# Kernel tuning notes

Hardware: AMD Instinct MI355X
Metric: run time of the kernel (lower is better)

Reference implementation:

```python
import jax, jax.numpy as jnp
import numpy as np

BOUND = 3.0
MIN_BIN_W = 1e-3   # min_bin_width
MIN_BIN_H = 1e-3   # min_bin_height
MIN_DERIV = 1e-3   # min_derivative
MIN_LAMBDA = 0.025
EPS = 1e-6


def _knots(frac, min_size, left, right):
    # frac: [D, K] normalized (softmax) bin fractions -> (bin sizes [D,K], knot positions [D,K+1])
    K = frac.shape[-1]
    sizes = min_size + (1.0 - min_size * K) * frac
    cum = jnp.cumsum(sizes, axis=-1)
    cum = jnp.concatenate([jnp.zeros_like(cum[..., :1]), cum], axis=-1)
    cum = (right - left) * cum + left
    cum = cum.at[..., 0].set(left)
    cum = cum.at[..., -1].set(right)
    sizes = cum[..., 1:] - cum[..., :-1]
    return sizes, cum


def _spline_fwd(x, uw, uh, ud, ul, bound=BOUND):
    # x: [B, D]; uw/uh/ul: [D, K]; ud: [D, K-1]
    B, D = x.shape
    K = uw.shape[-1]
    w = jax.nn.softmax(uw, axis=-1)
    h = jax.nn.softmax(uh, axis=-1)
    d = MIN_DERIV + jax.nn.softplus(ud)
    lam = MIN_LAMBDA + (1.0 - 2.0 * MIN_LAMBDA) * jax.nn.sigmoid(ul)

    left, right = -bound, bound
    widths, cumwidths = _knots(w, MIN_BIN_W, left, right)
    heights, cumheights = _knots(h, MIN_BIN_H, left, right)
    ones = jnp.ones_like(d[..., :1])
    derivs = jnp.concatenate([ones, d, ones], axis=-1)  # [D, K+1]; identity slope at the tails

    inside = (x >= left) & (x <= right)
    xc = jnp.clip(x, left, right)  # keep spline branch NaN-free for outside points

    # bucketize: index of bin containing each input, per dimension  -> [B, D]
    bin_idx = jnp.sum(xc[..., None] >= (cumwidths + EPS)[None], axis=-1) - 1
    bin_idx = jnp.clip(bin_idx, 0, K - 1)

    def sel(t):
        # gather per-(sample, dim) bin parameter: t [D, K or K+1] -> [B, D]
        tb = jnp.broadcast_to(t[None], (B,) + t.shape)
        return jnp.take_along_axis(tb, bin_idx[..., None], axis=-1)[..., 0]

    iw, icw = sel(widths), sel(cumwidths)
    ih, ich = sel(heights), sel(cumheights)
    idelta = sel(heights / widths)
    d0, d1 = sel(derivs), sel(derivs[..., 1:])
    il = sel(lam)

    # monotonic *linear* rational spline (Dolatabadi et al.), forward direction
    wa = 1.0
    wb = jnp.sqrt(d0 / d1) * wa
    wc = (il * wa * d0 + (1.0 - il) * wb * d1) / idelta
    ya = ich
    yb = ih + ich
    yc = ((1.0 - il) * wa * ya + il * wb * yb) / ((1.0 - il) * wa + il * wb)

    theta = (xc - icw) / iw
    lo = theta <= il
    num = jnp.where(lo,
                    wa * ya * (il - theta) + wc * yc * theta,
                    wc * yc * (1.0 - theta) + wb * yb * (theta - il))
    den = jnp.where(lo,
                    wa * (il - theta) + wc * theta,
                    wc * (1.0 - theta) + wb * (theta - il))
    dnum = jnp.where(lo,
                     wa * wc * il * (yc - ya),
                     wb * wc * (1.0 - il) * (yb - yc)) / iw

    u = jnp.where(inside, num / den, x)                      # identity outside the box
    logabsdet = jnp.where(inside, jnp.log(dnum) - 2.0 * jnp.log(jnp.abs(den)), 0.0)
    return u, jnp.sum(logabsdet, axis=1)


def setup_inputs() -> dict:
    B, D, K = 32768, 256, 32
    key = jax.random.key(0)
    k1, k2, k3, k4, k5 = jax.random.split(key, 5)
    return {
        "x": jax.random.normal(k1, (B, D), jnp.float32),
        "uw": jax.random.normal(k2, (D, K), jnp.float32),
        "uh": jax.random.normal(k3, (D, K), jnp.float32),
        "ud": jax.random.normal(k4, (D, K - 1), jnp.float32),
        "ul": jax.random.uniform(k5, (D, K), jnp.float32),
    }


def reference(x, uw, uh, ud, ul):
    # f: data x -> latent u, plus log|det J| summed over feature dim
    return _spline_fwd(x, uw, uh, ud, ul)
```

## Files before the change

### kernel.cpp

```cpp
#include <hip/hip_runtime.h>
#include <hip/hip_fp16.h>
#include <math.h>
#include <stdint.h>

#define D_DIM 256
#define K_BINS 32
#define NCELL 1024
#define ENT_DW 8
#define ENT_STRIDE 260
#define LIC_STRIDE 34
#define LUT_BSTRIDE 1028
#define SLICE 16

static constexpr float BOUND = 3.0f;
static constexpr float MIN_BIN_W = 1e-3f;
static constexpr float MIN_DERIV = 1e-3f;
static constexpr float MIN_LAMBDA = 0.025f;
static constexpr float EPS_ = 1e-6f;
static constexpr float CELL_W = 6.0f / NCELL;
static constexpr float CELL_S = NCELL / 6.0f;
static constexpr float LN2_ = 0.69314718055994531f;

__device__ __forceinline__ float softplusf_(float x) {
  return fmaxf(x, 0.0f) + log1pf(expf(-fabsf(x)));
}

__device__ __forceinline__ float pack2h_as_f32(float a, float b) {
  __half2 h = __halves2half2(__float2half_rn(a), __float2half_rn(b));
  union { __half2 h; uint32_t u; } c;
  c.h = h;
  return __uint_as_float(c.u);
}

__device__ __forceinline__ float2 unpack2h_from_f32(float v) {
  union { uint32_t u; __half2 h; } c;
  c.u = __float_as_uint(v);
  return make_float2(__low2float(c.h), __high2float(c.h));
}

__device__ __forceinline__ float dpp_rowsum16(float v) {
  int t;
  t = __builtin_amdgcn_update_dpp(0, __float_as_int(v), 0x128, 0xF, 0xF, false);
  v += __int_as_float(t);
  t = __builtin_amdgcn_update_dpp(0, __float_as_int(v), 0x124, 0xF, 0xF, false);
  v += __int_as_float(t);
  t = __builtin_amdgcn_update_dpp(0, __float_as_int(v), 0x122, 0xF, 0xF, false);
  v += __int_as_float(t);
  t = __builtin_amdgcn_update_dpp(0, __float_as_int(v), 0x121, 0xF, 0xF, false);
  v += __int_as_float(t);
  return v;
}

__global__ __launch_bounds__(512) void spline_fused(
    const float* __restrict__ x,
    const float* __restrict__ uw,
    const float* __restrict__ uh,
    const float* __restrict__ ud,
    const float* __restrict__ ul,
    float* __restrict__ uout,
    float* __restrict__ part,
    int B) {
  __shared__ float lent[SLICE * ENT_STRIDE];
  __shared__ float lic[SLICE * LIC_STRIDE];
  __shared__ uint8_t lutb[SLICE * LUT_BSTRIDE];

  int tid = threadIdx.x;
  int slice = blockIdx.x & 15;
  int group = blockIdx.x >> 4;
  int d0 = slice * SLICE;

  {
    int k = tid & 31;
    int dim = tid >> 5;
    int d = d0 + dim;

    float uwv = uw[d * K_BINS + k];
    float uhv = uh[d * K_BINS + k];
    float ulv = ul[d * K_BINS + k];
    float udv = (k < K_BINS - 1) ? ud[d * (K_BINS - 1) + k] : 0.0f;

    float wm = uwv, hm = uhv;
    for (int o = 16; o; o >>= 1) {
      wm = fmaxf(wm, __shfl_xor(wm, o, 32));
      hm = fmaxf(hm, __shfl_xor(hm, o, 32));
    }
    float ew = expf(uwv - wm), eh = expf(uhv - hm);
    float ws = ew, hs = eh;
    for (int o = 16; o; o >>= 1) {
      ws += __shfl_xor(ws, o, 32);
      hs += __shfl_xor(hs, o, 32);
    }
    const float kfac = 1.0f - MIN_BIN_W * (float)K_BINS;
    float sw = MIN_BIN_W + kfac * (ew / ws);
    float sh = MIN_BIN_W + kfac * (eh / hs);

    float cws = sw, chs = sh;
    for (int o = 1; o < 32; o <<= 1) {
      float tw = __shfl_up(cws, o, 32);
      float th = __shfl_up(chs, o, 32);
      if (k >= o) { cws += tw; chs += th; }
    }
    const float scale = 2.0f * BOUND;
    float raw_w = scale * cws - BOUND;
    float raw_h = scale * chs - BOUND;
    float upw = __shfl_up(raw_w, 1, 32);
    float uph = __shfl_up(raw_h, 1, 32);
    float cw_lo = (k == 0) ? -BOUND : upw;
    float ch_lo = (k == 0) ? -BOUND : uph;
    float cw_hi = (k == K_BINS - 1) ? BOUND : raw_w;
    float ch_hi = (k == K_BINS - 1) ? BOUND : raw_h;

    float iw = cw_hi - cw_lo;
    float ih = ch_hi - ch_lo;

    float dk = MIN_DERIV + softplusf_(udv);
    float dprev = __shfl_up(dk, 1, 32);
    float d1 = (k == K_BINS - 1) ? 1.0f : dk;
    float dd0 = (k == 0) ? 1.0f : dprev;

    float sg = 1.0f / (1.0f + expf(-ulv));
    float lam = MIN_LAMBDA + (1.0f - 2.0f * MIN_LAMBDA) * sg;

    float wb = sqrtf(dd0 / d1);
    float delta = ih / iw;
    float wc = (lam * dd0 + (1.0f - lam) * wb * d1) / delta;
    float denom = (1.0f - lam) + lam * wb;
    float dyc = lam * wb * ih / denom;
    float dyb = ih - dyc;
    float ya = ch_lo;
    float inv_iw = 1.0f / iw;
    float yc = ya + dyc;

    float* e = &lent[dim * ENT_STRIDE + k * ENT_DW];
    e[0] = cw_lo;
    e[1] = inv_iw;
    e[2] = lam;
    e[3] = wc;
    e[4] = wb;
    e[5] = yc;
    e[6] = pack2h_as_f32(dyc, dyb);
    e[7] = pack2h_as_f32(log2f(wc * lam * dyc * inv_iw),
                         log2f(wc * wb * (1.0f - lam) * dyb * inv_iw));

    float t = cw_lo + EPS_;
    lic[dim * LIC_STRIDE + k] = t;
    if (k == 0) lic[dim * LIC_STRIDE + 32] = 1e30f;

    int c0 = 0;
    if (k > 0) {
      float q = (t + BOUND + 1e-5f) * CELL_S;
      c0 = (int)ceilf(q);
      if (c0 < 0) c0 = 0;
      if (c0 > NCELL) c0 = NCELL;
      while (c0 < NCELL && (fmaf((float)c0, CELL_W, -BOUND) - 1e-5f) < t) ++c0;
      while (c0 > 0 && (fmaf((float)(c0 - 1), CELL_W, -BOUND) - 1e-5f) >= t) --c0;
    }
    int c1 = __shfl_down(c0, 1, 32);
    if (k == K_BINS - 1) c1 = NCELL;
    for (int c = c0; c < c1; ++c) lutb[dim * LUT_BSTRIDE + c] = (uint8_t)k;
  }
  __syncthreads();

  int lane = tid & 63;
  int wid = tid >> 6;
  int r4 = lane >> 4;
  int dsl = lane & 15;

  int row0 = group * 32 + wid * 4 + r4;
  size_t base = (size_t)row0 * D_DIM + d0 + dsl;
  const int entb = dsl * ENT_STRIDE;
  const int licb = dsl * LIC_STRIDE;
  const int lutbase = dsl * LUT_BSTRIDE;
  float* parts = part + (size_t)slice * B;

  int niter = B >> 11;
  for (int it = 0; it < niter; ++it) {
    int row = row0 + (it << 11);
    size_t gidx = base + ((size_t)it << 11) * D_DIM;

    float xv = x[gidx];
    float xc = fminf(fmaxf(xv, -BOUND), BOUND);
    bool inside = fabsf(xv) <= BOUND;

    float cf = fmaf(xc, CELL_S, (float)(NCELL / 2));
    int c = (int)cf;
    c = min(c, NCELL - 1);
    int ilut = (int)lutb[lutbase + c];

    float c1 = lic[licb + ilut + 1];
    int idx = ilut + (xc >= c1 ? 1 : 0);

    int eb = entb + idx * ENT_DW;
    float4 A = *reinterpret_cast<const float4*>(&lent[eb]);
    float4 Bv = *reinterpret_cast<const float4*>(&lent[eb + 4]);

    float icw = A.x, inv_iw = A.y, il = A.z, wcv = A.w;
    float wbv = Bv.x, yc = Bv.y;
    float2 dd = unpack2h_from_f32(Bv.z);
    float2 LL = unpack2h_from_f32(Bv.w);

    float theta = (xc - icw) * inv_iw;
    bool lo = theta <= il;
    float t1 = il - theta;
    float t3 = 1.0f - theta;

    float den = lo ? fmaf(wcv, theta, t1)
                   : fmaf(wcv, t3, -(wbv * t1));
    float sfac = lo ? dd.x : (wbv * dd.y);
    float Ls = lo ? LL.x : LL.y;

    float r = __builtin_amdgcn_rcpf(den);
    float uu = fmaf(-t1 * sfac, r, yc);
    float lad2 = fmaf(-2.0f, __builtin_amdgcn_logf(den), Ls);

    uout[gidx] = inside ? uu : xv;
    float ls = inside ? lad2 : 0.0f;

    ls = dpp_rowsum16(ls);
    if (dsl == 0) parts[row] = ls;
  }
}

__global__ void spline_reduce(const float* __restrict__ part,
                              float* __restrict__ ldout, int B) {
  int row = blockIdx.x * 256 + threadIdx.x;
  if (row >= B) return;
  float s = 0.0f;
#pragma unroll
  for (int sl = 0; sl < D_DIM / SLICE; ++sl) s += part[(size_t)sl * B + row];
  ldout[row] = s * LN2_;
}

extern "C" void kernel_launch(void* const* d_in, const int* in_sizes, int n_in,
                              void* d_out, int out_size, void* d_ws, size_t ws_size,
                              hipStream_t stream) {
  const float* x  = (const float*)d_in[0];
  const float* uw = (const float*)d_in[1];
  const float* uh = (const float*)d_in[2];
  const float* ud = (const float*)d_in[3];
  const float* ul = (const float*)d_in[4];

  int B = in_sizes[0] / D_DIM;

  float* out = (float*)d_out;
  float* uout = out;
  float* ldout = out + (size_t)B * D_DIM;

  float* partw = (float*)d_ws;

  spline_fused<<<1024, 512, 0, stream>>>(x, uw, uh, ud, ul, uout, partw, B);
  spline_reduce<<<(B + 255) / 256, 256, 0, stream>>>(partw, ldout, B);
}
```

Measured before the change: 32.40 us.

## Vectorize spline evaluation to four dims per lane with software-prefetched float4 loads

Each lane now handles four consecutive feature dims through float4 loads and stores, instead of one scalar element per iteration. The row loop is fully unrolled to four iterations, and the next x vector is prefetched while the current one is evaluated. The per-row log-det reduction now sums inside each lane and then across a 4-lane quad with DPP, instead of a 16-lane row sum. The loop count is now fixed for B=32768, and the LDS access pattern changes: fewer distinct dims are read per instruction, which can raise bank conflicts on the table lookups.

```diff
diff --git a/kernel.cpp b/kernel.cpp
--- a/kernel.cpp
+++ b/kernel.cpp
@@ -38,17 +38,55 @@
   return make_float2(__low2float(c.h), __high2float(c.h));
 }
 
-__device__ __forceinline__ float dpp_rowsum16(float v) {
+__device__ __forceinline__ float dpp_quadsum4(float v) {
   int t;
-  t = __builtin_amdgcn_update_dpp(0, __float_as_int(v), 0x128, 0xF, 0xF, false);
+  t = __builtin_amdgcn_update_dpp(0, __float_as_int(v), 0xB1, 0xF, 0xF, false);
   v += __int_as_float(t);
-  t = __builtin_amdgcn_update_dpp(0, __float_as_int(v), 0x124, 0xF, 0xF, false);
-  v += __int_as_float(t);
-  t = __builtin_amdgcn_update_dpp(0, __float_as_int(v), 0x122, 0xF, 0xF, false);
-  v += __int_as_float(t);
-  t = __builtin_amdgcn_update_dpp(0, __float_as_int(v), 0x121, 0xF, 0xF, false);
+  t = __builtin_amdgcn_update_dpp(0, __float_as_int(v), 0x4E, 0xF, 0xF, false);
   v += __int_as_float(t);
   return v;
+}
+
+__device__ __forceinline__ void eval1(
+    float xv, int dml,
+    const float* lent, const float* lic, const uint8_t* lutb,
+    float& uu_out, float& lad2_out) {
+  float xc = fminf(fmaxf(xv, -BOUND), BOUND);
+  bool inside = fabsf(xv) <= BOUND;
+
+  float cf = fmaf(xc, CELL_S, (float)(NCELL / 2));
+  int c = (int)cf;
+  c = min(c, NCELL - 1);
+  int ilut = (int)lutb[dml * LUT_BSTRIDE + c];
+
+  float c1 = lic[dml * LIC_STRIDE + ilut + 1];
+  int idx = ilut + (xc >= c1 ? 1 : 0);
+
+  int eb = dml * ENT_STRIDE + idx * ENT_DW;
+  float4 A = *reinterpret_cast<const float4*>(&lent[eb]);
+  float4 Bv = *reinterpret_cast<const float4*>(&lent[eb + 4]);
+
+  float icw = A.x, inv_iw = A.y, il = A.z, wcv = A.w;
+  float wbv = Bv.x, yc = Bv.y;
+  float2 dd = unpack2h_from_f32(Bv.z);
+  float2 LL = unpack2h_from_f32(Bv.w);
+
+  float theta = (xc - icw) * inv_iw;
+  bool lo = theta <= il;
+  float t1 = il - theta;
+  float t3 = 1.0f - theta;
+
+  float den = lo ? fmaf(wcv, theta, t1)
+                 : fmaf(wcv, t3, -(wbv * t1));
+  float sfac = lo ? dd.x : (wbv * dd.y);
+  float Ls = lo ? LL.x : LL.y;
+
+  float r = __builtin_amdgcn_rcpf(den);
+  float uu = fmaf(-t1 * sfac, r, yc);
+  float lad2 = fmaf(-2.0f, __builtin_amdgcn_logf(den), Ls);
+
+  uu_out = inside ? uu : xv;
+  lad2_out = inside ? lad2 : 0.0f;
 }
 
 __global__ __launch_bounds__(512) void spline_fused(
@@ -163,61 +201,36 @@
 
   int lane = tid & 63;
   int wid = tid >> 6;
-  int r4 = lane >> 4;
-  int dsl = lane & 15;
-
-  int row0 = group * 32 + wid * 4 + r4;
-  size_t base = (size_t)row0 * D_DIM + d0 + dsl;
-  const int entb = dsl * ENT_STRIDE;
-  const int licb = dsl * LIC_STRIDE;
-  const int lutbase = dsl * LUT_BSTRIDE;
+  int dq = lane & 3;
+  int rsub = lane >> 2;
+  int dml0 = dq * 4;
+
+  int row0 = group * 512 + wid * 16 + rsub;
+  size_t base = (size_t)row0 * D_DIM + d0 + dml0;
   float* parts = part + (size_t)slice * B;
-
-  int niter = B >> 11;
-  for (int it = 0; it < niter; ++it) {
-    int row = row0 + (it << 11);
-    size_t gidx = base + ((size_t)it << 11) * D_DIM;
-
-    float xv = x[gidx];
-    float xc = fminf(fmaxf(xv, -BOUND), BOUND);
-    bool inside = fabsf(xv) <= BOUND;
-
-    float cf = fmaf(xc, CELL_S, (float)(NCELL / 2));
-    int c = (int)cf;
-    c = min(c, NCELL - 1);
-    int ilut = (int)lutb[lutbase + c];
-
-    float c1 = lic[licb + ilut + 1];
-    int idx = ilut + (xc >= c1 ? 1 : 0);
-
-    int eb = entb + idx * ENT_DW;
-    float4 A = *reinterpret_cast<const float4*>(&lent[eb]);
-    float4 Bv = *reinterpret_cast<const float4*>(&lent[eb + 4]);
-
-    float icw = A.x, inv_iw = A.y, il = A.z, wcv = A.w;
-    float wbv = Bv.x, yc = Bv.y;
-    float2 dd = unpack2h_from_f32(Bv.z);
-    float2 LL = unpack2h_from_f32(Bv.w);
-
-    float theta = (xc - icw) * inv_iw;
-    bool lo = theta <= il;
-    float t1 = il - theta;
-    float t3 = 1.0f - theta;
-
-    float den = lo ? fmaf(wcv, theta, t1)
-                   : fmaf(wcv, t3, -(wbv * t1));
-    float sfac = lo ? dd.x : (wbv * dd.y);
-    float Ls = lo ? LL.x : LL.y;
-
-    float r = __builtin_amdgcn_rcpf(den);
-    float uu = fmaf(-t1 * sfac, r, yc);
-    float lad2 = fmaf(-2.0f, __builtin_amdgcn_logf(den), Ls);
-
-    uout[gidx] = inside ? uu : xv;
-    float ls = inside ? lad2 : 0.0f;
-
-    ls = dpp_rowsum16(ls);
-    if (dsl == 0) parts[row] = ls;
+  const size_t ISTEP = (size_t)128 * D_DIM;
+
+  float4 xv = *reinterpret_cast<const float4*>(x + base);
+
+#pragma unroll
+  for (int it = 0; it < 4; ++it) {
+    float4 xn;
+    if (it < 3) xn = *reinterpret_cast<const float4*>(x + base + (size_t)(it + 1) * ISTEP);
+
+    float u0, u1, u2, u3, l0, l1, l2, l3;
+    eval1(xv.x, dml0 + 0, lent, lic, lutb, u0, l0);
+    eval1(xv.y, dml0 + 1, lent, lic, lutb, u1, l1);
+    eval1(xv.z, dml0 + 2, lent, lic, lutb, u2, l2);
+    eval1(xv.w, dml0 + 3, lent, lic, lutb, u3, l3);
+
+    float4 uv = make_float4(u0, u1, u2, u3);
+    *reinterpret_cast<float4*>(uout + base + (size_t)it * ISTEP) = uv;
+
+    float ls = (l0 + l1) + (l2 + l3);
+    ls = dpp_quadsum4(ls);
+    if (dq == 0) parts[row0 + it * 128] = ls;
+
+    xv = xn;
   }
 }
 
```

Result: faster. 29.30 us (-9.6%).
